# Performance work log

Hardware: AMD Instinct MI355X
Metric: run time of the kernel (lower is better)

## Reference

```python
import jax, jax.numpy as jnp
import numpy as np

B, C, H, W = 8, 256, 64, 64
E, D, K = 4, 4, 2
CR = C // 16  # CBAM channel-attention reduction ratio 16

def _conv(x, w, pad):
    return jax.lax.conv_general_dilated(
        x, w, (1, 1), [(pad, pad), (pad, pad)],
        dimension_numbers=('NCHW', 'OIHW', 'NCHW'))

def _bn(x, s, b):  # eval-mode BatchNorm folded into per-channel affine
    return x * s[None, :, None, None] + b[None, :, None, None]

def _expert(p, x, dom_ids):
    # domain_transform: conv3x3-BN-GELU-conv3x3-BN
    h = jax.nn.gelu(_bn(_conv(x, p['dt_w1'], 1), p['dt_bn1s'], p['dt_bn1b']))
    d = _bn(_conv(h, p['dt_w2'], 1), p['dt_bn2s'], p['dt_bn2b'])
    # domain_gate: GAP -> conv1x1 C->1 -> sigmoid
    g1 = jax.nn.sigmoid(jnp.mean(d, (2, 3)) @ p['gate_w'] + p['gate_b'])  # [B]
    out = x + g1[:, None, None, None] * d
    # Res_CBAM_block (in==out channels, stride 1 -> identity shortcut)
    r = out
    h = jax.nn.relu(_bn(_conv(out, p['c1_w'], 1) + p['c1_b'][None, :, None, None], p['bn1s'], p['bn1b']))
    h = _bn(_conv(h, p['c2_w'], 1) + p['c2_b'][None, :, None, None], p['bn2s'], p['bn2b'])
    # channel attention (shared MLP over GAP and GMP)
    avg, mx = jnp.mean(h, (2, 3)), jnp.max(h, (2, 3))
    mlp = lambda v: jax.nn.relu(v @ p['ca_w1'].T) @ p['ca_w2'].T
    ca = jax.nn.sigmoid(mlp(avg) + mlp(mx))  # [B,C]
    h = h * ca[:, :, None, None]
    # spatial attention: 7x7 conv over [mean_c, max_c]
    sa_in = jnp.concatenate([jnp.mean(h, 1, keepdims=True), jnp.max(h, 1, keepdims=True)], axis=1)
    sa = jax.nn.sigmoid(_conv(sa_in, p['sa_w'], 3))
    h = jax.nn.relu(h * sa + r)
    # per-domain adapter bias (nn.Embedding lookup)
    return h + p['adp'][dom_ids][:, :, None, None]

def _forward(x, domain_ids, g_w1, g_b1, ln_s, ln_b, g_w2, g_b2, dom_emb,
             e_dt_w1, e_dt_bn1s, e_dt_bn1b, e_dt_w2, e_dt_bn2s, e_dt_bn2b,
             e_gate_w, e_gate_b, e_c1_w, e_c1_b, e_bn1s, e_bn1b,
             e_c2_w, e_c2_b, e_bn2s, e_bn2b, e_ca_w1, e_ca_w2, e_sa_w, e_adapter):
    ep = dict(dt_w1=e_dt_w1, dt_bn1s=e_dt_bn1s, dt_bn1b=e_dt_bn1b,
              dt_w2=e_dt_w2, dt_bn2s=e_dt_bn2s, dt_bn2b=e_dt_bn2b,
              gate_w=e_gate_w, gate_b=e_gate_b,
              c1_w=e_c1_w, c1_b=e_c1_b, bn1s=e_bn1s, bn1b=e_bn1b,
              c2_w=e_c2_w, c2_b=e_c2_b, bn2s=e_bn2s, bn2b=e_bn2b,
              ca_w1=e_ca_w1, ca_w2=e_ca_w2, sa_w=e_sa_w, adp=e_adapter)
    eouts = jax.vmap(_expert, in_axes=(0, None, None))(ep, x, domain_ids)  # [E,B,C,H,W]
    # gate input: [GAP(x) | GMP(x) | domain_embed(16)] -> Linear -> LN -> ReLU -> Linear -> softmax
    gi = jnp.concatenate([jnp.mean(x, (2, 3)), jnp.max(x, (2, 3)), dom_emb[domain_ids]], axis=1)
    hg = gi @ g_w1 + g_b1
    mu = jnp.mean(hg, -1, keepdims=True)
    var = jnp.var(hg, -1, keepdims=True)
    hg = jax.nn.relu((hg - mu) * jax.lax.rsqrt(var + 1e-5) * ln_s + ln_b)
    probs = jax.nn.softmax(hg @ g_w2 + g_b2, axis=-1)  # [B,E]
    vals, idx = jax.lax.top_k(probs, K)                # soft top-k routing
    wk = vals / jnp.sum(vals, -1, keepdims=True)       # renormalize top-k weights
    wfull = jnp.zeros_like(probs).at[jnp.arange(probs.shape[0])[:, None], idx].set(wk)
    return jnp.einsum('be,ebchw->bchw', wfull, eouts)

def setup_inputs():
    key = jax.random.key(0)
    ks = iter(jax.random.split(key, 48))
    rn = lambda shape, s=0.05: jax.random.normal(next(ks), shape, jnp.float32) * s
    p = {}
    p['x'] = jax.random.normal(next(ks), (B, C, H, W), jnp.float32)
    p['domain_ids'] = jax.random.randint(next(ks), (B,), 0, D)
    p['g_w1'] = rn((2 * C + 16, C)); p['g_b1'] = jnp.zeros((C,))
    p['ln_s'] = jnp.ones((C,)); p['ln_b'] = jnp.zeros((C,))
    p['g_w2'] = rn((C, E)); p['g_b2'] = jnp.zeros((E,))
    p['dom_emb'] = rn((D, 16), 0.5)
    p['e_dt_w1'] = rn((E, C, C, 3, 3)); p['e_dt_bn1s'] = jnp.ones((E, C)); p['e_dt_bn1b'] = jnp.zeros((E, C))
    p['e_dt_w2'] = rn((E, C, C, 3, 3)); p['e_dt_bn2s'] = jnp.ones((E, C)); p['e_dt_bn2b'] = jnp.zeros((E, C))
    p['e_gate_w'] = rn((E, C)); p['e_gate_b'] = jnp.zeros((E,))
    p['e_c1_w'] = rn((E, C, C, 3, 3)); p['e_c1_b'] = jnp.zeros((E, C))
    p['e_bn1s'] = jnp.ones((E, C)); p['e_bn1b'] = jnp.zeros((E, C))
    p['e_c2_w'] = rn((E, C, C, 3, 3)); p['e_c2_b'] = jnp.zeros((E, C))
    p['e_bn2s'] = jnp.ones((E, C)); p['e_bn2b'] = jnp.zeros((E, C))
    p['e_ca_w1'] = rn((E, CR, C)); p['e_ca_w2'] = rn((E, C, CR))
    p['e_sa_w'] = rn((E, 1, 2, 7, 7))
    p['e_adapter'] = rn((E, D, C), 0.1)
    return p

def reference(x, domain_ids, g_w1, g_b1, ln_s, ln_b, g_w2, g_b2, dom_emb,
              e_dt_w1, e_dt_bn1s, e_dt_bn1b, e_dt_w2, e_dt_bn2s, e_dt_bn2b,
              e_gate_w, e_gate_b, e_c1_w, e_c1_b, e_bn1s, e_bn1b,
              e_c2_w, e_c2_b, e_bn2s, e_bn2b, e_ca_w1, e_ca_w2, e_sa_w, e_adapter):
    return _forward(x, domain_ids, g_w1, g_b1, ln_s, ln_b, g_w2, g_b2, dom_emb,
                    e_dt_w1, e_dt_bn1s, e_dt_bn1b, e_dt_w2, e_dt_bn2s, e_dt_bn2b,
                    e_gate_w, e_gate_b, e_c1_w, e_c1_b, e_bn1s, e_bn1b,
                    e_c2_w, e_c2_b, e_bn2s, e_bn2b, e_ca_w1, e_ca_w2, e_sa_w, e_adapter)
```

## Files before the change

kernel.cpp:

```cpp
#include <hip/hip_runtime.h>
#include <math.h>

typedef __bf16 bf16x8 __attribute__((ext_vector_type(8)));
typedef float  f32x4  __attribute__((ext_vector_type(4)));

#define NB 8
#define NC 256
#define NHW 4096
#define NCHW_ 1048576
#define NSLOT 16

__device__ __forceinline__ float sigmoidf_(float x){ return 1.f/(1.f+expf(-x)); }
__device__ __forceinline__ float gelu_tanh(float x){
  float x3 = x*x*x;
  return 0.5f*x*(1.f+tanhf(0.7978845608028654f*(x + 0.044715f*x3)));
}

__device__ __forceinline__ void gload16(const void* g, void* l){
  __builtin_amdgcn_global_load_lds((const __attribute__((address_space(1))) void*)g,
                                   (__attribute__((address_space(3))) void*)l,
                                   16, 0, 0);
}

__global__ void k_prep_sb(const float* dt_bn1s, const float* dt_bn1b,
                          const float* dt_bn2s, const float* dt_bn2b,
                          const float* c1_b, const float* bn1s, const float* bn1b,
                          const float* c2_b, const float* bn2s, const float* bn2b,
                          float* effS, float* effB){
  int ec = blockIdx.x; int e = ec>>2, cv = ec&3; int c = threadIdx.x;
  int i = e*NC + c;
  float s, b;
  if (cv==0){ s = dt_bn1s[i]; b = dt_bn1b[i]; }
  else if (cv==1){ s = dt_bn2s[i]; b = dt_bn2b[i]; }
  else if (cv==2){ s = bn1s[i]; b = c1_b[i]*bn1s[i] + bn1b[i]; }
  else { s = bn2s[i]; b = c2_b[i]*bn2s[i] + bn2b[i]; }
  effS[ec*NC+c]=s; effB[ec*NC+c]=b;
}

__global__ void k_prep_w(const float* w0, const float* w1, const float* w2, const float* w3,
                         __bf16* wr){
  __shared__ float tl[9][257];
  int o = blockIdx.x; int ec = blockIdx.y; int e = ec>>2, cv = ec&3;
  int t = threadIdx.x;
  const float* src = (cv==0)?w0 : (cv==1)?w1 : (cv==2)?w2 : w3;
  const float* sp = src + ((size_t)((e*NC + o)*NC + t))*9;
  #pragma unroll
  for (int k=0;k<9;k++) tl[k][t] = sp[k];
  __syncthreads();
  __bf16* dst = wr + (size_t)ec*589824 + (size_t)o*256;
  #pragma unroll
  for (int k=0;k<9;k++) dst[(size_t)k*65536 + t] = (__bf16)tl[k][t];
}

__global__ void k_prep_x(const float* x, __bf16* xh, float* gps, float* gpm){
  __shared__ float tl[32][33];
  __shared__ float rs[256], rm[256];
  int ptile = blockIdx.x, p0 = ptile*32, c0 = blockIdx.y*32, b = blockIdx.z;
  int tx = threadIdx.x&31, ty = threadIdx.x>>5;
  #pragma unroll
  for (int k=0;k<4;k++){
    int c = c0 + ty + k*8;
    tl[ty+k*8][tx] = x[(size_t)(b*NC+c)*NHW + p0 + tx];
  }
  __syncthreads();
  #pragma unroll
  for (int k=0;k<4;k++){
    int p = p0 + ty + k*8;
    xh[(size_t)b*NCHW_ + (size_t)p*NC + c0 + tx] = (__bf16)tl[tx][ty+k*8];
  }
  int c_local = threadIdx.x & 31, seg = threadIdx.x >> 5;
  float s=0.f, m=-1e30f;
  #pragma unroll
  for (int j=0;j<4;j++){ float v = tl[c_local][seg*4+j]; s+=v; m=fmaxf(m,v); }
  rs[seg*32+c_local]=s; rm[seg*32+c_local]=m;
  __syncthreads();
  if (threadIdx.x < 32){
    float ss=0.f, mm=-1e30f;
    #pragma unroll
    for (int g=0; g<8; g++){ ss += rs[g*32+threadIdx.x]; mm = fmaxf(mm, rm[g*32+threadIdx.x]); }
    gps[(size_t)(b*128+ptile)*256 + c0 + threadIdx.x] = ss;
    gpm[(size_t)(b*128+ptile)*256 + c0 + threadIdx.x] = mm;
  }
}

__global__ void k_gate1b(const float* gps, const float* gpm, float* gavg, float* gmax){
  int b = blockIdx.x, c = threadIdx.x;
  float s=0.f, m=-1e30f;
  for (int k=0;k<128;k++){
    s += gps[(size_t)(b*128+k)*256 + c];
    m = fmaxf(m, gpm[(size_t)(b*128+k)*256 + c]);
  }
  gavg[b*256+c] = s/4096.f;
  gmax[b*256+c] = m;
}

__global__ void k_gate2(const float* gavg, const float* gmax, const int* dom,
                        const float* dom_emb, const float* w1, const float* b1,
                        const float* lns, const float* lnb,
                        const float* w2, const float* b2,
                        int* slot_e, float* slot_w){
  __shared__ float giT[528][8];
  __shared__ float hg[8][256];
  __shared__ float stat[16];
  __shared__ float logit[8][4];
  int t = threadIdx.x;
  for (int idx=t; idx<8*528; idx+=256){
    int b = idx&7, k = idx>>3;
    float v;
    if (k<256) v = gavg[b*256+k];
    else if (k<512) v = gmax[b*256+k-256];
    else v = dom_emb[dom[b]*16 + (k-512)];
    giT[k][b]=v;
  }
  __syncthreads();
  {
    float acc[8];
    float bb = b1[t];
    #pragma unroll
    for (int b=0;b<8;b++) acc[b]=bb;
    for (int k=0;k<528;k++){
      float wv = w1[k*256+t];
      #pragma unroll
      for (int b=0;b<8;b++) acc[b] += giT[k][b]*wv;
    }
    #pragma unroll
    for (int b=0;b<8;b++) hg[b][t]=acc[b];
  }
  __syncthreads();
  if (t<8){
    float mu=0.f; for(int c=0;c<256;c++) mu += hg[t][c]; mu/=256.f;
    float vr=0.f; for(int c=0;c<256;c++){ float d=hg[t][c]-mu; vr+=d*d; } vr/=256.f;
    stat[t]=mu; stat[8+t]=vr;
  }
  __syncthreads();
  for (int b=0;b<8;b++){
    float v = (hg[b][t]-stat[b])*rsqrtf(stat[8+b]+1e-5f)*lns[t]+lnb[t];
    hg[b][t] = fmaxf(v, 0.f);
  }
  __syncthreads();
  if (t<32){
    int b = t>>2, e = t&3;
    float acc = b2[e];
    for (int c=0;c<256;c++) acc += hg[b][c]*w2[c*4+e];
    logit[b][e]=acc;
  }
  __syncthreads();
  if (t==0){
    for (int b=0;b<8;b++){
      float mx = logit[b][0];
      for (int e=1;e<4;e++) mx = fmaxf(mx, logit[b][e]);
      float p[4], s=0.f;
      for (int e=0;e<4;e++){ p[e]=expf(logit[b][e]-mx); s+=p[e]; }
      for (int e=0;e<4;e++) p[e]/=s;
      int i0=0; for (int e=1;e<4;e++) if (p[e]>p[i0]) i0=e;
      int i1=-1; for (int e=0;e<4;e++){ if (e==i0) continue; if (i1<0 || p[e]>p[i1]) i1=e; }
      float den = p[i0]+p[i1];
      slot_e[2*b]   = i0; slot_w[2*b]   = p[i0]/den;
      slot_e[2*b+1] = i1; slot_w[2*b+1] = p[i1]/den;
    }
  }
}

template<int ACT, int RED>
__global__ __launch_bounds__(256,2) void k_conv(
    const __bf16* __restrict__ in0, int per_b,
    const __bf16* __restrict__ wr,  int conv_idx,
    const float* __restrict__ effS, const float* __restrict__ effB,
    const int* __restrict__ slot_e,
    const __bf16* __restrict__ zslab,
    __bf16* __restrict__ out,
    const float* __restrict__ gate_w, float* __restrict__ p_sum,
    float* __restrict__ ca_ps, float* __restrict__ ca_pm)
{
  __shared__ __bf16 smem[17408];
  __bf16* lA = smem;
  __bf16* lB = smem + 8192;

  const int tid   = threadIdx.x;
  const int lin   = blockIdx.y*64 + blockIdx.x;
  const int xcd   = lin & 7;
  const int q     = lin >> 3;
  const int slot  = (xcd<<1) | (q>>6);
  const int t64   = q & 63;
  const int tileM = t64 & 1;
  const int tileN = t64 >> 1;
  const int e     = slot_e[slot];
  const int cout_base = tileM*128;
  const int pos_base  = tileN*128;
  const int lane   = tid & 63;
  const int wv     = tid >> 6;
  const int lane15 = lane & 15, quad = lane >> 4;
  const int m_off  = (wv&1)*64, n_off = (wv>>1)*64;

  const __bf16* in = in0 + (size_t)(per_b ? (slot>>1) : slot) * NCHW_;
  const __bf16* wb = wr + (size_t)(e*4 + conv_idx) * 589824;

  int ldsOff[4];
  int aOff[4];
  int bBase[4];
  int rr0[4], cl0[4];
  #pragma unroll
  for (int j=0;j<4;j++){
    int f = (wv*4+j)*64 + lane;
    int row = f>>3, ph = f&7;
    int lc = ph ^ (row&7);
    ldsOff[j] = f*8;
    aOff[j]   = (cout_base + row)*256 + lc*8;
    int gp = pos_base + row;
    rr0[j] = gp>>6; cl0[j] = gp&63;
    bBase[j] = lc*8;
  }

  f32x4 zero = {0.f,0.f,0.f,0.f};
  f32x4 acc[4][4];
  #pragma unroll
  for (int i=0;i<4;i++)
    #pragma unroll
    for (int j=0;j<4;j++) acc[i][j] = zero;

  const int ph_read = lane15 & 7;

  for (int kk=0; kk<36; ++kk){
    const int k9 = kk>>2, c0e = (kk&3)*64;
    const int k3 = k9/3;
    const int dy = k3 - 1, dx = k9 - k3*3 - 1;
    __syncthreads();
    {
      const __bf16* ws = wb + (size_t)k9*65536 + c0e;
      #pragma unroll
      for (int j=0;j<4;j++)
        gload16(ws + aOff[j], lA + ldsOff[j]);
    }
    {
      const int doff = dy*16384 + dx*256 + c0e;
      #pragma unroll
      for (int j=0;j<4;j++){
        int rr = rr0[j] + dy, cl = cl0[j] + dx;
        const __bf16* src = ((unsigned)rr < 64u && (unsigned)cl < 64u)
            ? in + (size_t)(rr0[j]*16384 + cl0[j]*256 + doff + bBase[j])
            : zslab;
        gload16(src, lB + ldsOff[j]);
      }
    }
    __syncthreads();
    #pragma unroll
    for (int s=0;s<2;s++){
      bf16x8 af[4], bfr[4];
      const int ph = (s*4 + quad) ^ ph_read;
      #pragma unroll
      for (int i=0;i<4;i++) af[i]  = *(const bf16x8*)(lA + (m_off + i*16 + lane15)*64 + ph*8);
      #pragma unroll
      for (int j=0;j<4;j++) bfr[j] = *(const bf16x8*)(lB + (n_off + j*16 + lane15)*64 + ph*8);
      #pragma unroll
      for (int i=0;i<4;i++)
        #pragma unroll
        for (int j=0;j<4;j++)
          acc[i][j] = __builtin_amdgcn_mfma_f32_16x16x32_bf16(af[i], bfr[j], acc[i][j], 0,0,0);
    }
  }
  __syncthreads();

  const float* sS = effS + (e*4+conv_idx)*256 + cout_base;
  const float* sB = effB + (e*4+conv_idx)*256 + cout_base;
  float sc[16], bi[16];
  #pragma unroll
  for (int i=0;i<4;i++)
    #pragma unroll
    for (int r=0;r<4;r++){
      int m = m_off + i*16 + quad*4 + r;
      sc[i*4+r] = sS[m]; bi[i*4+r] = sB[m];
    }
  __bf16* lO = smem;
  #pragma unroll
  for (int i=0;i<4;i++){
    #pragma unroll
    for (int j=0;j<4;j++){
      int n = n_off + j*16 + lane15;
      #pragma unroll
      for (int r=0;r<4;r++){
        int m = m_off + i*16 + quad*4 + r;
        float v = acc[i][j][r]*sc[i*4+r] + bi[i*4+r];
        if (ACT==1) v = gelu_tanh(v);
        if (ACT==2) v = fmaxf(v, 0.f);
        lO[n*136 + m] = (__bf16)v;
      }
    }
  }
  __syncthreads();
  __bf16* ob = out + (size_t)slot*NCHW_;
  #pragma unroll
  for (int h=0; h<8; ++h){
    int chunk = tid + h*256;
    int prow = chunk>>4, part = chunk&15;
    *(uint4*)(ob + (size_t)(pos_base+prow)*256 + cout_base + part*8) =
      *(const uint4*)(lO + prow*136 + part*8);
  }

  if (RED==1){
    int m = tid & 127, half = tid >> 7;
    float s = 0.f;
    const __bf16* col = lO + (half*64)*136 + m;
    #pragma unroll 8
    for (int n=0;n<64;n++) s += (float)col[n*136];
    s *= gate_w[e*256 + cout_base + m];
    #pragma unroll
    for (int off=32; off; off>>=1) s += __shfl_down(s, off);
    __syncthreads();
    float* scr = (float*)smem;
    if (lane==0) scr[wv] = s;
    __syncthreads();
    if (tid==0) p_sum[slot*64 + tileN*2 + tileM] = scr[0]+scr[1]+scr[2]+scr[3];
  }
  if (RED==2){
    int m = tid & 127, half = tid >> 7;
    float s=0.f, mx=-1e30f;
    const __bf16* col = lO + (half*64)*136 + m;
    #pragma unroll 8
    for (int n=0;n<64;n++){ float v = (float)col[n*136]; s+=v; mx=fmaxf(mx,v); }
    __syncthreads();
    float* scr = (float*)smem;
    scr[half*128+m] = s; scr[256 + half*128+m] = mx;
    __syncthreads();
    if (tid<128){
      float ts = scr[tid] + scr[128+tid];
      float tm = fmaxf(scr[256+tid], scr[384+tid]);
      ca_ps[(size_t)(slot*32+tileN)*256 + cout_base + tid] = ts;
      ca_pm[(size_t)(slot*32+tileN)*256 + cout_base + tid] = tm;
    }
  }
}

__global__ void k_g1fin(const float* p_sum, const float* gate_b, const int* slot_e, float* g1s){
  int t = threadIdx.x;
  if (t<16){
    float s=0.f;
    for (int k=0;k<64;k++) s += p_sum[t*64+k];
    g1s[t] = sigmoidf_(s/4096.f + gate_b[slot_e[t]]);
  }
}

__global__ void k_pw_r(const __bf16* xh, const __bf16* d, const float* g1s, __bf16* r){
  int slot = blockIdx.y;
  int idx = blockIdx.x*256 + threadIdx.x;
  float g1 = g1s[slot];
  size_t o = (size_t)slot*NCHW_ + idx;
  r[o] = (__bf16)((float)xh[(size_t)(slot>>1)*NCHW_ + idx] + g1*(float)d[o]);
}

__global__ void k_ca2(const float* ps, const float* pm, const float* w1, const float* w2,
                      const int* slot_e, float* ca){
  __shared__ float avg[256], mxs[256], hr[32];
  int slot = blockIdx.x, t = threadIdx.x;
  int e = slot_e[slot];
  float s=0.f, m=-1e30f;
  #pragma unroll
  for (int k=0;k<32;k++){
    s += ps[(size_t)(slot*32+k)*256+t];
    m = fmaxf(m, pm[(size_t)(slot*32+k)*256+t]);
  }
  avg[t]=s/4096.f; mxs[t]=m;
  __syncthreads();
  if (t<32){
    int j = t&15; int which = t>>4;
    const float* v = which? mxs : avg;
    float acc=0.f;
    for (int c=0;c<256;c++) acc += v[c]*w1[e*4096 + j*256 + c];
    hr[t] = fmaxf(acc, 0.f);
  }
  __syncthreads();
  float acc=0.f;
  #pragma unroll
  for (int j=0;j<16;j++) acc += (hr[j]+hr[16+j])*w2[e*4096 + t*16 + j];
  ca[slot*256+t] = sigmoidf_(acc);
}

__global__ void k_sa1(const __bf16* h3, const float* ca, float* sam){
  int slot = blockIdx.y;
  int wv = threadIdx.x>>6, lane = threadIdx.x&63;
  int p = blockIdx.x*4 + wv;
  const __bf16* base = h3 + (size_t)slot*NCHW_ + (size_t)p*256 + lane*4;
  const float* cb = ca + slot*256 + lane*4;
  float s=0.f, m=-1e30f;
  #pragma unroll
  for (int k=0;k<4;k++){ float v = (float)base[k]*cb[k]; s+=v; m=fmaxf(m,v); }
  #pragma unroll
  for (int off=32; off; off>>=1){ s += __shfl_down(s, off); m = fmaxf(m, __shfl_down(m, off)); }
  if (lane==0){ sam[slot*8192 + p] = s/256.f; sam[slot*8192 + 4096 + p] = m; }
}

__global__ void k_sa2(const float* sam, const float* sa_w, const int* slot_e, float* sa){
  int slot = blockIdx.y;
  int p = blockIdx.x*256 + threadIdx.x;
  int e = slot_e[slot];
  int y = p>>6, x = p&63;
  const float* m0 = sam + slot*8192;
  const float* m1 = m0 + 4096;
  const float* w = sa_w + e*98;
  float acc = 0.f;
  for (int ky=0;ky<7;ky++){
    int yy = y + ky - 3;
    if ((unsigned)yy >= 64u) continue;
    for (int kx=0;kx<7;kx++){
      int xx = x + kx - 3;
      if ((unsigned)xx >= 64u) continue;
      acc += w[ky*7+kx]*m0[yy*64+xx] + w[49+ky*7+kx]*m1[yy*64+xx];
    }
  }
  sa[slot*4096+p] = sigmoidf_(acc);
}

__global__ void k_fin(const __bf16* h3, const __bf16* r, const float* ca, const float* sa,
                      const int* slot_e, const float* slot_w, const float* adapter,
                      const int* dom, float* out){
  __shared__ float tl[32][33];
  int p0 = blockIdx.x*32, c0 = blockIdx.y*32, b = blockIdx.z;
  int tx = threadIdx.x&31, ty = threadIdx.x>>5;
  int s0 = b*2, s1 = b*2+1;
  int e0 = slot_e[s0], e1 = slot_e[s1];
  float w0 = slot_w[s0], w1 = slot_w[s1];
  int dm = dom[b];
  int c = c0 + tx;
  float ad = w0*adapter[(e0*4+dm)*256 + c] + w1*adapter[(e1*4+dm)*256 + c];
  float ca0 = ca[s0*256+c], ca1 = ca[s1*256+c];
  #pragma unroll
  for (int k=0;k<4;k++){
    int p = p0 + ty + k*8;
    size_t o0 = (size_t)s0*NCHW_ + (size_t)p*256 + c;
    size_t o1 = (size_t)s1*NCHW_ + (size_t)p*256 + c;
    float v0 = (float)h3[o0]*ca0*sa[s0*4096+p] + (float)r[o0];
    float v1 = (float)h3[o1]*ca1*sa[s1*4096+p] + (float)r[o1];
    tl[tx][ty+k*8] = w0*fmaxf(v0,0.f) + w1*fmaxf(v1,0.f) + ad;
  }
  __syncthreads();
  #pragma unroll
  for (int k=0;k<4;k++){
    int cc = c0 + ty + k*8;
    out[((size_t)(b*NC+cc))*NHW + p0 + tx] = tl[ty+k*8][tx];
  }
}

extern "C" void kernel_launch(void* const* d_in, const int* in_sizes, int n_in,
                              void* d_out, int out_size, void* d_ws, size_t ws_size,
                              hipStream_t stream){
  const float* x      = (const float*)d_in[0];
  const int*   dom    = (const int*)d_in[1];
  const float* g_w1   = (const float*)d_in[2];
  const float* g_b1   = (const float*)d_in[3];
  const float* ln_s   = (const float*)d_in[4];
  const float* ln_b   = (const float*)d_in[5];
  const float* g_w2   = (const float*)d_in[6];
  const float* g_b2   = (const float*)d_in[7];
  const float* dom_emb= (const float*)d_in[8];
  const float* dt_w1  = (const float*)d_in[9];
  const float* dt_bn1s= (const float*)d_in[10];
  const float* dt_bn1b= (const float*)d_in[11];
  const float* dt_w2  = (const float*)d_in[12];
  const float* dt_bn2s= (const float*)d_in[13];
  const float* dt_bn2b= (const float*)d_in[14];
  const float* gate_w = (const float*)d_in[15];
  const float* gate_b = (const float*)d_in[16];
  const float* c1_w   = (const float*)d_in[17];
  const float* c1_b   = (const float*)d_in[18];
  const float* bn1s   = (const float*)d_in[19];
  const float* bn1b   = (const float*)d_in[20];
  const float* c2_w   = (const float*)d_in[21];
  const float* c2_b   = (const float*)d_in[22];
  const float* bn2s   = (const float*)d_in[23];
  const float* bn2b   = (const float*)d_in[24];
  const float* ca_w1  = (const float*)d_in[25];
  const float* ca_w2  = (const float*)d_in[26];
  const float* sa_w   = (const float*)d_in[27];
  const float* adapter= (const float*)d_in[28];

  char* ws = (char*)d_ws;
  size_t off = 0;
  auto alloc = [&](size_t bytes)->void*{
    void* p = ws + off; off += (bytes + 255) & ~size_t(255); return p;
  };
  __bf16* wr   = (__bf16*)alloc(16ull*589824*2);
  __bf16* xh   = (__bf16*)alloc(8ull*NCHW_*2);
  __bf16* bufA = (__bf16*)alloc(16ull*NCHW_*2);
  __bf16* bufB = (__bf16*)alloc(16ull*NCHW_*2);
  __bf16* bufC = (__bf16*)alloc(16ull*NCHW_*2);
  float* gps   = (float*)alloc(8ull*128*256*4);
  float* gpm   = (float*)alloc(8ull*128*256*4);
  float* gavg  = (float*)alloc(2048*4);
  float* gmax  = (float*)alloc(2048*4);
  float* effS  = (float*)alloc(4096*4);
  float* effB  = (float*)alloc(4096*4);
  int*   slot_e= (int*)alloc(64);
  float* slot_w= (float*)alloc(64);
  float* p_sum = (float*)alloc(16*64*4);
  float* g1s   = (float*)alloc(64);
  float* ca_ps = (float*)alloc(16*32*256*4);
  float* ca_pm = (float*)alloc(16*32*256*4);
  float* ca    = (float*)alloc(16*256*4);
  float* sam   = (float*)alloc(16*8192*4);
  float* sa    = (float*)alloc(16*4096*4);
  __bf16* zslab= (__bf16*)alloc(512);

  hipMemsetAsync(zslab, 0, 512, stream);

  k_prep_sb<<<dim3(16), dim3(256), 0, stream>>>(dt_bn1s, dt_bn1b, dt_bn2s, dt_bn2b,
                                                c1_b, bn1s, bn1b, c2_b, bn2s, bn2b, effS, effB);
  k_prep_w<<<dim3(256,16), dim3(256), 0, stream>>>(dt_w1, dt_w2, c1_w, c2_w, wr);
  k_prep_x<<<dim3(128,8,8), dim3(256), 0, stream>>>(x, xh, gps, gpm);
  k_gate1b<<<dim3(8), dim3(256), 0, stream>>>(gps, gpm, gavg, gmax);
  k_gate2<<<dim3(1), dim3(256), 0, stream>>>(gavg, gmax, dom, dom_emb, g_w1, g_b1,
                                             ln_s, ln_b, g_w2, g_b2, slot_e, slot_w);
  k_conv<1,0><<<dim3(64,16), dim3(256), 0, stream>>>(xh, 1, wr, 0, effS, effB, slot_e, zslab, bufA,
                                                     gate_w, p_sum, ca_ps, ca_pm);
  k_conv<0,1><<<dim3(64,16), dim3(256), 0, stream>>>(bufA, 0, wr, 1, effS, effB, slot_e, zslab, bufB,
                                                     gate_w, p_sum, ca_ps, ca_pm);
  k_g1fin<<<dim3(1), dim3(64), 0, stream>>>(p_sum, gate_b, slot_e, g1s);
  k_pw_r<<<dim3(4096,16), dim3(256), 0, stream>>>(xh, bufB, g1s, bufC);
  k_conv<2,0><<<dim3(64,16), dim3(256), 0, stream>>>(bufC, 0, wr, 2, effS, effB, slot_e, zslab, bufA,
                                                     gate_w, p_sum, ca_ps, ca_pm);
  k_conv<0,2><<<dim3(64,16), dim3(256), 0, stream>>>(bufA, 0, wr, 3, effS, effB, slot_e, zslab, bufB,
                                                     gate_w, p_sum, ca_ps, ca_pm);
  k_ca2<<<dim3(16), dim3(256), 0, stream>>>(ca_ps, ca_pm, ca_w1, ca_w2, slot_e, ca);
  k_sa1<<<dim3(1024,16), dim3(256), 0, stream>>>(bufB, ca, sam);
  k_sa2<<<dim3(16,16), dim3(256), 0, stream>>>(sam, sa_w, slot_e, sa);
  k_fin<<<dim3(128,8,8), dim3(256), 0, stream>>>(bufB, bufC, ca, sa, slot_e, slot_w,
                                                 adapter, dom, (float*)d_out);
}
```

Baseline: 615.6 us.

## Reuse haloed input tile across conv taps, fuse gate and spatial-attention kernels

```diff
diff --git a/kernel.cpp b/kernel.cpp
--- a/kernel.cpp
+++ b/kernel.cpp
@@ -162,7 +162,7 @@
 }
 
 template<int ACT, int RED>
-__global__ __launch_bounds__(256,2) void k_conv(
+__global__ __launch_bounds__(256,3) void k_conv(
     const __bf16* __restrict__ in0, int per_b,
     const __bf16* __restrict__ wr,  int conv_idx,
     const float* __restrict__ effS, const float* __restrict__ effB,
@@ -172,9 +172,9 @@
     const float* __restrict__ gate_w, float* __restrict__ p_sum,
     float* __restrict__ ca_ps, float* __restrict__ ca_pm)
 {
-  __shared__ __bf16 smem[17408];
-  __bf16* lA = smem;
-  __bf16* lB = smem + 8192;
+  __shared__ __bf16 smem[24576];
+  __bf16* lBH = smem;
+  __bf16* lA  = smem + 16384;
 
   const int tid   = threadIdx.x;
   const int lin   = blockIdx.y*64 + blockIdx.x;
@@ -195,20 +195,22 @@
   const __bf16* in = in0 + (size_t)(per_b ? (slot>>1) : slot) * NCHW_;
   const __bf16* wb = wr + (size_t)(e*4 + conv_idx) * 589824;
 
-  int ldsOff[4];
-  int aOff[4];
-  int bBase[4];
-  int rr0[4], cl0[4];
-  #pragma unroll
-  for (int j=0;j<4;j++){
-    int f = (wv*4+j)*64 + lane;
+  int bOff[8];
+  #pragma unroll
+  for (int j=0;j<8;j++){
+    int f = j*256 + tid;
     int row = f>>3, ph = f&7;
     int lc = ph ^ (row&7);
-    ldsOff[j] = f*8;
-    aOff[j]   = (cout_base + row)*256 + lc*8;
-    int gp = pos_base + row;
-    rr0[j] = gp>>6; cl0[j] = gp&63;
-    bBase[j] = lc*8;
+    int pos = pos_base - 64 + row;
+    bOff[j] = ((unsigned)pos < 4096u) ? pos*256 + lc*8 : -1;
+  }
+  int aOff[4];
+  #pragma unroll
+  for (int j=0;j<4;j++){
+    int f = j*256 + tid;
+    int row = f>>3, ph = f&7;
+    int lc = ph ^ (row&7);
+    aOff[j] = (cout_base + row)*256 + lc*8;
   }
 
   f32x4 zero = {0.f,0.f,0.f,0.f};
@@ -218,44 +220,52 @@
     #pragma unroll
     for (int j=0;j<4;j++) acc[i][j] = zero;
 
-  const int ph_read = lane15 & 7;
-
-  for (int kk=0; kk<36; ++kk){
-    const int k9 = kk>>2, c0e = (kk&3)*64;
-    const int k3 = k9/3;
-    const int dy = k3 - 1, dx = k9 - k3*3 - 1;
+  bf16x8 zfrag;
+  #pragma unroll
+  for (int k=0;k<8;k++) zfrag[k] = (__bf16)0.f;
+
+  #pragma unroll 1
+  for (int ch=0; ch<4; ++ch){
+    const int c0e = ch*64;
     __syncthreads();
-    {
-      const __bf16* ws = wb + (size_t)k9*65536 + c0e;
+    #pragma unroll
+    for (int j=0;j<8;j++){
+      const __bf16* src = (bOff[j] >= 0) ? (in + bOff[j] + c0e) : zslab;
+      gload16(src, lBH + (j*256+tid)*8);
+    }
+    #pragma unroll
+    for (int tap=0; tap<9; ++tap){
+      const int dy = tap/3 - 1, dx = tap - (tap/3)*3 - 1;
+      if (tap) __syncthreads();
+      {
+        const __bf16* ws = wb + (size_t)tap*65536 + c0e;
+        #pragma unroll
+        for (int j=0;j<4;j++) gload16(ws + aOff[j], lA + (j*256+tid)*8);
+      }
+      __syncthreads();
+      const int xr = (lane15 + dx) & 7;
+      const int rb = 64 + dy*64 + dx + lane15;
       #pragma unroll
-      for (int j=0;j<4;j++)
-        gload16(ws + aOff[j], lA + ldsOff[j]);
-    }
-    {
-      const int doff = dy*16384 + dx*256 + c0e;
-      #pragma unroll
-      for (int j=0;j<4;j++){
-        int rr = rr0[j] + dy, cl = cl0[j] + dx;
-        const __bf16* src = ((unsigned)rr < 64u && (unsigned)cl < 64u)
-            ? in + (size_t)(rr0[j]*16384 + cl0[j]*256 + doff + bBase[j])
-            : zslab;
-        gload16(src, lB + ldsOff[j]);
+      for (int s=0;s<2;s++){
+        const int kc = s*4 + quad;
+        const int aph = (kc ^ (lane15&7))*8;
+        const int bph = (kc ^ xr)*8;
+        bf16x8 af[4], bfr[4];
+        #pragma unroll
+        for (int i=0;i<4;i++) af[i] = *(const bf16x8*)(lA + (m_off + i*16 + lane15)*64 + aph);
+        #pragma unroll
+        for (int j=0;j<4;j++){
+          int rrow = (n_off + j*16 + rb) & 255;
+          bfr[j] = *(const bf16x8*)(lBH + rrow*64 + bph);
+        }
+        if (dx==-1 && lane15==0)  bfr[0] = zfrag;
+        if (dx==1  && lane15==15) bfr[3] = zfrag;
+        #pragma unroll
+        for (int i=0;i<4;i++)
+          #pragma unroll
+          for (int j=0;j<4;j++)
+            acc[i][j] = __builtin_amdgcn_mfma_f32_16x16x32_bf16(af[i], bfr[j], acc[i][j], 0,0,0);
       }
-    }
-    __syncthreads();
-    #pragma unroll
-    for (int s=0;s<2;s++){
-      bf16x8 af[4], bfr[4];
-      const int ph = (s*4 + quad) ^ ph_read;
-      #pragma unroll
-      for (int i=0;i<4;i++) af[i]  = *(const bf16x8*)(lA + (m_off + i*16 + lane15)*64 + ph*8);
-      #pragma unroll
-      for (int j=0;j<4;j++) bfr[j] = *(const bf16x8*)(lB + (n_off + j*16 + lane15)*64 + ph*8);
-      #pragma unroll
-      for (int i=0;i<4;i++)
-        #pragma unroll
-        for (int j=0;j<4;j++)
-          acc[i][j] = __builtin_amdgcn_mfma_f32_16x16x32_bf16(af[i], bfr[j], acc[i][j], 0,0,0);
     }
   }
   __syncthreads();
@@ -330,21 +340,20 @@
   }
 }
 
-__global__ void k_g1fin(const float* p_sum, const float* gate_b, const int* slot_e, float* g1s){
-  int t = threadIdx.x;
-  if (t<16){
-    float s=0.f;
-    for (int k=0;k<64;k++) s += p_sum[t*64+k];
-    g1s[t] = sigmoidf_(s/4096.f + gate_b[slot_e[t]]);
-  }
-}
-
-__global__ void k_pw_r(const __bf16* xh, const __bf16* d, const float* g1s, __bf16* r){
+__global__ void k_pw_r(const __bf16* xh, const __bf16* d, const float* p_sum,
+                       const float* gate_b, const int* slot_e, __bf16* r){
   int slot = blockIdx.y;
-  int idx = blockIdx.x*256 + threadIdx.x;
-  float g1 = g1s[slot];
-  size_t o = (size_t)slot*NCHW_ + idx;
-  r[o] = (__bf16)((float)xh[(size_t)(slot>>1)*NCHW_ + idx] + g1*(float)d[o]);
+  float tot = 0.f;
+  #pragma unroll
+  for (int k=0;k<64;k++) tot += p_sum[slot*64+k];
+  float g1 = sigmoidf_(tot/4096.f + gate_b[slot_e[slot]]);
+  size_t idx8 = ((size_t)blockIdx.x*256 + threadIdx.x)*8;
+  bf16x8 xv = *(const bf16x8*)(xh + (size_t)(slot>>1)*NCHW_ + idx8);
+  bf16x8 dv = *(const bf16x8*)(d + (size_t)slot*NCHW_ + idx8);
+  bf16x8 rv;
+  #pragma unroll
+  for (int k=0;k<8;k++) rv[k] = (__bf16)((float)xv[k] + g1*(float)dv[k]);
+  *(bf16x8*)(r + (size_t)slot*NCHW_ + idx8) = rv;
 }
 
 __global__ void k_ca2(const float* ps, const float* pm, const float* w1, const float* w2,
@@ -388,55 +397,59 @@
   if (lane==0){ sam[slot*8192 + p] = s/256.f; sam[slot*8192 + 4096 + p] = m; }
 }
 
-__global__ void k_sa2(const float* sam, const float* sa_w, const int* slot_e, float* sa){
-  int slot = blockIdx.y;
-  int p = blockIdx.x*256 + threadIdx.x;
-  int e = slot_e[slot];
-  int y = p>>6, x = p&63;
-  const float* m0 = sam + slot*8192;
-  const float* m1 = m0 + 4096;
-  const float* w = sa_w + e*98;
-  float acc = 0.f;
-  for (int ky=0;ky<7;ky++){
-    int yy = y + ky - 3;
-    if ((unsigned)yy >= 64u) continue;
-    for (int kx=0;kx<7;kx++){
-      int xx = x + kx - 3;
-      if ((unsigned)xx >= 64u) continue;
-      acc += w[ky*7+kx]*m0[yy*64+xx] + w[49+ky*7+kx]*m1[yy*64+xx];
-    }
-  }
-  sa[slot*4096+p] = sigmoidf_(acc);
-}
-
-__global__ void k_fin(const __bf16* h3, const __bf16* r, const float* ca, const float* sa,
-                      const int* slot_e, const float* slot_w, const float* adapter,
-                      const int* dom, float* out){
-  __shared__ float tl[32][33];
-  int p0 = blockIdx.x*32, c0 = blockIdx.y*32, b = blockIdx.z;
-  int tx = threadIdx.x&31, ty = threadIdx.x>>5;
-  int s0 = b*2, s1 = b*2+1;
-  int e0 = slot_e[s0], e1 = slot_e[s1];
-  float w0 = slot_w[s0], w1 = slot_w[s1];
-  int dm = dom[b];
-  int c = c0 + tx;
-  float ad = w0*adapter[(e0*4+dm)*256 + c] + w1*adapter[(e1*4+dm)*256 + c];
-  float ca0 = ca[s0*256+c], ca1 = ca[s1*256+c];
-  #pragma unroll
-  for (int k=0;k<4;k++){
-    int p = p0 + ty + k*8;
-    size_t o0 = (size_t)s0*NCHW_ + (size_t)p*256 + c;
-    size_t o1 = (size_t)s1*NCHW_ + (size_t)p*256 + c;
-    float v0 = (float)h3[o0]*ca0*sa[s0*4096+p] + (float)r[o0];
-    float v1 = (float)h3[o1]*ca1*sa[s1*4096+p] + (float)r[o1];
-    tl[tx][ty+k*8] = w0*fmaxf(v0,0.f) + w1*fmaxf(v1,0.f) + ad;
-  }
-  __syncthreads();
-  #pragma unroll
-  for (int k=0;k<4;k++){
-    int cc = c0 + ty + k*8;
-    out[((size_t)(b*NC+cc))*NHW + p0 + tx] = tl[ty+k*8][tx];
-  }
+__global__ void k_fin(const __bf16* h3, const __bf16* r, const float* ca, const float* sam,
+                      const float* sa_w, const int* slot_e, const float* slot_w,
+                      const float* adapter, const int* dom, float* out){
+  __shared__ float tl[64][33];
+  __shared__ float sAtt[2][32];
+  const int p0 = blockIdx.x*32, c0 = blockIdx.y*64, b = blockIdx.z;
+  const int t = threadIdx.x;
+  const int s0 = b*2, s1 = s0+1;
+  if (t < 64){
+    int pp = p0 + (t&31);
+    int sl = s0 + (t>>5);
+    int e = slot_e[sl];
+    int y = pp>>6, x0 = pp&63;
+    const float* m0 = sam + sl*8192;
+    const float* m1 = m0 + 4096;
+    const float* w = sa_w + e*98;
+    float acc = 0.f;
+    for (int ky=0;ky<7;ky++){
+      int yy = y+ky-3; if ((unsigned)yy>=64u) continue;
+      for (int kx=0;kx<7;kx++){
+        int xx = x0+kx-3; if ((unsigned)xx>=64u) continue;
+        acc += w[ky*7+kx]*m0[yy*64+xx] + w[49+ky*7+kx]*m1[yy*64+xx];
+      }
+    }
+    sAtt[t>>5][t&31] = sigmoidf_(acc);
+  }
+  __syncthreads();
+  const int prow = t>>3;
+  const int cchunk = t&7;
+  const int pos = p0 + prow;
+  const int cb = c0 + cchunk*8;
+  const int e0 = slot_e[s0], e1 = slot_e[s1];
+  const float w0 = slot_w[s0], w1 = slot_w[s1];
+  const int dm = dom[b];
+  size_t o0 = (size_t)s0*NCHW_ + (size_t)pos*256 + cb;
+  size_t o1 = (size_t)s1*NCHW_ + (size_t)pos*256 + cb;
+  bf16x8 h0v = *(const bf16x8*)(h3+o0), h1v = *(const bf16x8*)(h3+o1);
+  bf16x8 r0v = *(const bf16x8*)(r+o0),  r1v = *(const bf16x8*)(r+o1);
+  float sa0 = sAtt[0][prow], sa1 = sAtt[1][prow];
+  #pragma unroll
+  for (int k=0;k<8;k++){
+    int c = cb + k;
+    float v0 = (float)h0v[k]*ca[s0*256+c]*sa0 + (float)r0v[k];
+    float v1 = (float)h1v[k]*ca[s1*256+c]*sa1 + (float)r1v[k];
+    float val = w0*(fmaxf(v0,0.f) + adapter[(e0*4+dm)*256+c])
+              + w1*(fmaxf(v1,0.f) + adapter[(e1*4+dm)*256+c]);
+    tl[cchunk*8+k][prow] = val;
+  }
+  __syncthreads();
+  const int cl = t>>2, px = (t&3)*8;
+  #pragma unroll
+  for (int k=0;k<8;k++)
+    out[((size_t)(b*NC + c0 + cl))*NHW + p0 + px + k] = tl[cl][px+k];
 }
 
 extern "C" void kernel_launch(void* const* d_in, const int* in_sizes, int n_in,
@@ -491,12 +504,10 @@
   int*   slot_e= (int*)alloc(64);
   float* slot_w= (float*)alloc(64);
   float* p_sum = (float*)alloc(16*64*4);
-  float* g1s   = (float*)alloc(64);
   float* ca_ps = (float*)alloc(16*32*256*4);
   float* ca_pm = (float*)alloc(16*32*256*4);
   float* ca    = (float*)alloc(16*256*4);
   float* sam   = (float*)alloc(16*8192*4);
-  float* sa    = (float*)alloc(16*4096*4);
   __bf16* zslab= (__bf16*)alloc(512);
 
   hipMemsetAsync(zslab, 0, 512, stream);
@@ -512,15 +523,13 @@
                                                      gate_w, p_sum, ca_ps, ca_pm);
   k_conv<0,1><<<dim3(64,16), dim3(256), 0, stream>>>(bufA, 0, wr, 1, effS, effB, slot_e, zslab, bufB,
                                                      gate_w, p_sum, ca_ps, ca_pm);
-  k_g1fin<<<dim3(1), dim3(64), 0, stream>>>(p_sum, gate_b, slot_e, g1s);
-  k_pw_r<<<dim3(4096,16), dim3(256), 0, stream>>>(xh, bufB, g1s, bufC);
+  k_pw_r<<<dim3(512,16), dim3(256), 0, stream>>>(xh, bufB, p_sum, gate_b, slot_e, bufC);
   k_conv<2,0><<<dim3(64,16), dim3(256), 0, stream>>>(bufC, 0, wr, 2, effS, effB, slot_e, zslab, bufA,
                                                      gate_w, p_sum, ca_ps, ca_pm);
   k_conv<0,2><<<dim3(64,16), dim3(256), 0, stream>>>(bufA, 0, wr, 3, effS, effB, slot_e, zslab, bufB,
                                                      gate_w, p_sum, ca_ps, ca_pm);
   k_ca2<<<dim3(16), dim3(256), 0, stream>>>(ca_ps, ca_pm, ca_w1, ca_w2, slot_e, ca);
   k_sa1<<<dim3(1024,16), dim3(256), 0, stream>>>(bufB, ca, sam);
-  k_sa2<<<dim3(16,16), dim3(256), 0, stream>>>(sam, sa_w, slot_e, sa);
-  k_fin<<<dim3(128,8,8), dim3(256), 0, stream>>>(bufB, bufC, ca, sa, slot_e, slot_w,
+  k_fin<<<dim3(128,4,8), dim3(256), 0, stream>>>(bufB, bufC, ca, sam, sa_w, slot_e, slot_w,
                                                  adapter, dom, (float*)d_out);
 }
```

Result: slower. 803.6 us (+30.5%).
